# Performance work log

Hardware: AMD Instinct MI355X
Metric: run time of the kernel (lower is better)

Reference implementation:

```python
import jax, jax.numpy as jnp
import numpy as np

B, S, D, H = 2, 2048, 1280, 16
DEPTH = D // H  # 80


def setup_inputs() -> dict:
    key = jax.random.key(0)
    ks = jax.random.split(key, 6)
    scale = 1.0 / np.sqrt(D)
    x = jax.random.normal(ks[0], (B, S, D), dtype=jnp.float32)
    # causal mask: 1.0 where attention is disallowed (strict upper triangle)
    mask = jnp.triu(jnp.ones((S, S), dtype=jnp.float32), k=1)
    Wq = jax.random.normal(ks[1], (D, D), dtype=jnp.float32) * scale
    Wk = jax.random.normal(ks[2], (D, D), dtype=jnp.float32) * scale
    Wv = jax.random.normal(ks[3], (D, D), dtype=jnp.float32) * scale
    Wo = jax.random.normal(ks[4], (D, D), dtype=jnp.float32) * scale
    z = jnp.zeros((D,), dtype=jnp.float32)
    return {"x": x, "mask": mask, "Wq": Wq, "bq": z, "Wk": Wk, "bk": z,
            "Wv": Wv, "bv": z, "Wo": Wo, "bo": z}


def _split_heads(t):
    # [B, S, D] -> [B, H, S, depth]
    return t.reshape(B, -1, H, DEPTH).transpose(0, 2, 1, 3)


def reference(x, mask, Wq, bq, Wk, bk, Wv, bv, Wo, bo):
    q = _split_heads(x @ Wq + bq)
    k = _split_heads(x @ Wk + bk)
    v = _split_heads(x @ Wv + bv)
    # scaled dot-product attention with additive (masked * -10000) logits
    logits = jnp.einsum("bhqd,bhkd->bhqk", q, k) / jnp.sqrt(
        jnp.asarray(DEPTH, dtype=jnp.float32))
    logits = logits + mask * -10000.0  # mask broadcasts over [B, H]
    attn = jax.nn.softmax(logits, axis=-1)
    ctx = jnp.einsum("bhqk,bhkd->bhqd", attn, v)
    ctx = ctx.transpose(0, 2, 1, 3).reshape(B, -1, D)  # merge heads
    return ctx @ Wo + bo
```

## Files before the change

kernel.cpp:

```cpp
#include <hip/hip_runtime.h>

typedef unsigned short u16;
typedef __bf16 bf16;
typedef __bf16 bf16x8 __attribute__((ext_vector_type(8)));
typedef unsigned short u16x8 __attribute__((ext_vector_type(8)));
typedef unsigned short u16x4 __attribute__((ext_vector_type(4)));
typedef float f32x4 __attribute__((ext_vector_type(4)));

constexpr int B_ = 2, S_ = 2048, D_ = 1280, H_ = 16, DEPTH_ = 80;
constexpr int M_ = B_ * S_;
constexpr int QR_ = 128;

__device__ inline u16 f2b(float f) { return __builtin_bit_cast(u16, (bf16)f); }

typedef __attribute__((address_space(1))) const void gvoid;
typedef __attribute__((address_space(3))) void lvoid;
__device__ inline void gl_lds16(const void* g, void* l) {
  __builtin_amdgcn_global_load_lds((gvoid*)g, (lvoid*)l, 16, 0, 0);
}

__global__ __launch_bounds__(256) void prep_k(const float* __restrict__ x,
                                              u16* __restrict__ xbf,
                                              u16* __restrict__ QK,
                                              const float* __restrict__ W0,
                                              const float* __restrict__ W1,
                                              const float* __restrict__ W2,
                                              const float* __restrict__ W3,
                                              u16* __restrict__ WT) {
  __shared__ u16 t[32][33];
  int bid = blockIdx.x, tid = threadIdx.x;
  if (bid < 2560) {
    int i0 = (bid * 256 + tid) * 8;
    u16x8 v;
#pragma unroll
    for (int j = 0; j < 8; ++j) v[j] = f2b(x[i0 + j]);
    *(u16x8*)(xbf + i0) = v;
  } else if (bid < 5632) {
    int c = (bid - 2560) * 256 + tid;
    int r = c / 6, k = c - r * 6;
    u16x8 z = {};
    *(u16x8*)(QK + (size_t)r * QR_ + 80 + k * 8) = z;
  } else {
    int tt = bid - 5632;
    int z = tt / 1600, w = tt - z * 1600;
    int x0 = (w % 40) * 32, y0 = (w / 40) * 32;
    const float* srcs[4] = {W0, W1, W2, W3};
    const float* W = srcs[z];
    u16* out = WT + (size_t)z * D_ * D_;
    int tx = tid & 31, ty = tid >> 5;
#pragma unroll
    for (int i = 0; i < 4; ++i)
      t[ty + 8 * i][tx] = f2b(W[(size_t)(y0 + ty + 8 * i) * D_ + x0 + tx]);
    __syncthreads();
#pragma unroll
    for (int i = 0; i < 4; ++i)
      out[(size_t)(x0 + ty + 8 * i) * D_ + y0 + tx] = t[tx][ty + 8 * i];
  }
}

struct GemmAcc {
  f32x4 acc[4][4];
};
__device__ inline void gemm_core(const u16* __restrict__ A,
                                 const u16* __restrict__ BT, int m0, int n0,
                                 u16* a_s, u16* b_s, GemmAcc& g) {
  int tid = threadIdx.x, lane = tid & 63, wave = tid >> 6;
  int quad = lane >> 4, l15 = lane & 15;
  int wm = wave >> 1, wn = wave & 1;
  int r4 = lane >> 2, c4 = (lane & 3) * 8;

  for (int k0 = 0; k0 < D_; k0 += 32) {
    __syncthreads();
#pragma unroll
    for (int j = 0; j < 2; ++j) {
      int ch = wave * 2 + j;
      gl_lds16(A + (size_t)(m0 + ch * 16 + r4) * D_ + k0 + c4, a_s + ch * 512);
      gl_lds16(BT + (size_t)(n0 + ch * 16 + r4) * D_ + k0 + c4, b_s + ch * 512);
    }
    __syncthreads();
    bf16x8 af[4], bfr[4];
#pragma unroll
    for (int mt = 0; mt < 4; ++mt)
      af[mt] = *(const bf16x8*)(a_s + (wm * 64 + mt * 16 + l15) * 32 + quad * 8);
#pragma unroll
    for (int nt = 0; nt < 4; ++nt)
      bfr[nt] = *(const bf16x8*)(b_s + (wn * 64 + nt * 16 + l15) * 32 + quad * 8);
#pragma unroll
    for (int mt = 0; mt < 4; ++mt)
#pragma unroll
      for (int nt = 0; nt < 4; ++nt)
        g.acc[mt][nt] = __builtin_amdgcn_mfma_f32_16x16x32_bf16(
            af[mt], bfr[nt], g.acc[mt][nt], 0, 0, 0);
  }
}

__global__ __launch_bounds__(256, 4) void gemm_out(const u16* __restrict__ A,
                                                   const u16* __restrict__ BT,
                                                   const float* __restrict__ bias,
                                                   float* __restrict__ out) {
  __shared__ __align__(16) u16 a_s[128 * 32];
  __shared__ __align__(16) u16 b_s[128 * 32];
  int lane = threadIdx.x & 63, wave = threadIdx.x >> 6;
  int quad = lane >> 4, l15 = lane & 15;
  int wm = wave >> 1, wn = wave & 1;
  int m0 = blockIdx.y * 128, n0 = blockIdx.x * 128;

  GemmAcc g = {};
  gemm_core(A, BT, m0, n0, a_s, b_s, g);

#pragma unroll
  for (int nt = 0; nt < 4; ++nt) {
    int col = n0 + wn * 64 + nt * 16 + l15;
    float bv = bias[col];
#pragma unroll
    for (int mt = 0; mt < 4; ++mt)
#pragma unroll
      for (int r = 0; r < 4; ++r) {
        int row = m0 + wm * 64 + mt * 16 + quad * 4 + r;
        out[(size_t)row * D_ + col] = g.acc[mt][nt][r] + bv;
      }
  }
}

__device__ inline void stage_half(const u16* __restrict__ gsrc, int half,
                                  u16* lbase, int wave, int lane) {
  int rl = lane >> 3, c8 = lane & 7;
  int sc = (c8 ^ rl) << 3;
#pragma unroll
  for (int i = 0; i < 2; ++i) {
    int j = half * 16 + wave * 2 + i;
    gl_lds16(gsrc + (size_t)(j * 8 + rl) * D_ + sc, lbase + j * 512);
  }
}

__device__ inline bf16x8 frd(const u16* b, int r, int g) {
  return *(const bf16x8*)(b + r * 64 + ((g ^ (r & 7)) << 3));
}

__global__ __launch_bounds__(512, 2) void gemm_qkv8(
    const u16* __restrict__ A, const u16* __restrict__ BT,
    const float* __restrict__ bq, const float* __restrict__ bk,
    const float* __restrict__ bv, u16* __restrict__ Qw, u16* __restrict__ Kw,
    u16* __restrict__ Vw) {
  __shared__ __align__(16) u16 AS[2][256 * 64];
  __shared__ __align__(16) u16 BS[2][256 * 64];
  constexpr int BK = 64, NT = D_ / BK;
  int tid = threadIdx.x, lane = tid & 63, wave = tid >> 6;
  int quad = lane >> 4, l15 = lane & 15;
  int wm = wave >> 2, wn = wave & 3;
  int bid = blockIdx.x;
  int sw = (bid & 7) * 30 + (bid >> 3);
  int by = sw / 15, bx = sw - by * 15;
  int m0 = by * 256, n0 = bx * 256;
  const u16* Ab = A + (size_t)m0 * D_;
  const u16* Bb = BT + (size_t)n0 * D_;

  f32x4 acc[8][4] = {};

  stage_half(Ab, 0, (u16*)AS[0], wave, lane);
  stage_half(Ab, 1, (u16*)AS[0], wave, lane);
  stage_half(Bb, 0, (u16*)BS[0], wave, lane);
  stage_half(Bb, 1, (u16*)BS[0], wave, lane);
  stage_half(Bb + BK, 0, (u16*)BS[1], wave, lane);
  stage_half(Bb + BK, 1, (u16*)BS[1], wave, lane);
  asm volatile("s_waitcnt vmcnt(4)" ::: "memory");
  __builtin_amdgcn_s_barrier();

  bf16x8 a[4][2], bl[2][2], bh[2][2];
  int ra = wm * 128 + l15, rb = wn * 64 + l15;

#pragma unroll 2
  for (int T = 0; T < NT; ++T) {
    const u16* Ac = AS[T & 1];
    const u16* Bc = BS[T & 1];
    u16* An = (u16*)AS[(T + 1) & 1];
    u16* Bcur = (u16*)BS[T & 1];

#pragma unroll
    for (int mt = 0; mt < 4; ++mt)
#pragma unroll
      for (int kh = 0; kh < 2; ++kh)
        a[mt][kh] = frd(Ac, ra + mt * 16, kh * 4 + quad);
#pragma unroll
    for (int nt = 0; nt < 2; ++nt)
#pragma unroll
      for (int kh = 0; kh < 2; ++kh)
        bl[nt][kh] = frd(Bc, rb + nt * 16, kh * 4 + quad);
    if (T + 1 < NT) stage_half(Ab + (size_t)(T + 1) * BK, 0, An, wave, lane);
    asm volatile("" ::: "memory");
    __builtin_amdgcn_s_barrier();
    __builtin_amdgcn_s_setprio(1);
#pragma unroll
    for (int mt = 0; mt < 4; ++mt)
#pragma unroll
      for (int nt = 0; nt < 2; ++nt)
#pragma unroll
        for (int kh = 0; kh < 2; ++kh)
          acc[mt][nt] = __builtin_amdgcn_mfma_f32_16x16x32_bf16(
              a[mt][kh], bl[nt][kh], acc[mt][nt], 0, 0, 0);
    __builtin_amdgcn_s_setprio(0);
    asm volatile("" ::: "memory");
    __builtin_amdgcn_s_barrier();

#pragma unroll
    for (int nt = 0; nt < 2; ++nt)
#pragma unroll
      for (int kh = 0; kh < 2; ++kh)
        bh[nt][kh] = frd(Bc, rb + 32 + nt * 16, kh * 4 + quad);
    if (T + 1 < NT) stage_half(Ab + (size_t)(T + 1) * BK, 1, An, wave, lane);
    asm volatile("" ::: "memory");
    __builtin_amdgcn_s_barrier();
    __builtin_amdgcn_s_setprio(1);
#pragma unroll
    for (int mt = 0; mt < 4; ++mt)
#pragma unroll
      for (int nt = 0; nt < 2; ++nt)
#pragma unroll
        for (int kh = 0; kh < 2; ++kh)
          acc[mt][nt + 2] = __builtin_amdgcn_mfma_f32_16x16x32_bf16(
              a[mt][kh], bh[nt][kh], acc[mt][nt + 2], 0, 0, 0);
    __builtin_amdgcn_s_setprio(0);
    asm volatile("" ::: "memory");
    __builtin_amdgcn_s_barrier();

#pragma unroll
    for (int mt = 0; mt < 4; ++mt)
#pragma unroll
      for (int kh = 0; kh < 2; ++kh)
        a[mt][kh] = frd(Ac, ra + 64 + mt * 16, kh * 4 + quad);
    if (T + 2 < NT) stage_half(Bb + (size_t)(T + 2) * BK, 0, Bcur, wave, lane);
    asm volatile("" ::: "memory");
    __builtin_amdgcn_s_barrier();
    __builtin_amdgcn_s_setprio(1);
#pragma unroll
    for (int mt = 0; mt < 4; ++mt)
#pragma unroll
      for (int nt = 0; nt < 2; ++nt)
#pragma unroll
        for (int kh = 0; kh < 2; ++kh)
          acc[mt + 4][nt + 2] = __builtin_amdgcn_mfma_f32_16x16x32_bf16(
              a[mt][kh], bh[nt][kh], acc[mt + 4][nt + 2], 0, 0, 0);
    __builtin_amdgcn_s_setprio(0);
    asm volatile("" ::: "memory");
    __builtin_amdgcn_s_barrier();

    if (T + 2 < NT) stage_half(Bb + (size_t)(T + 2) * BK, 1, Bcur, wave, lane);
    asm volatile("" ::: "memory");
    __builtin_amdgcn_s_barrier();
    __builtin_amdgcn_s_setprio(1);
#pragma unroll
    for (int mt = 0; mt < 4; ++mt)
#pragma unroll
      for (int nt = 0; nt < 2; ++nt)
#pragma unroll
        for (int kh = 0; kh < 2; ++kh)
          acc[mt + 4][nt] = __builtin_amdgcn_mfma_f32_16x16x32_bf16(
              a[mt][kh], bl[nt][kh], acc[mt + 4][nt], 0, 0, 0);
    __builtin_amdgcn_s_setprio(0);
    if (T < NT - 2)
      asm volatile("s_waitcnt vmcnt(4)" ::: "memory");
    else if (T == NT - 2)
      asm volatile("s_waitcnt vmcnt(0)" ::: "memory");
    asm volatile("" ::: "memory");
    __builtin_amdgcn_s_barrier();
  }

  int mat = n0 / D_;
  if (mat == 2) {
#pragma unroll
    for (int nt = 0; nt < 4; ++nt) {
      int co = n0 + wn * 64 + nt * 16 + l15 - 2 * D_;
      float bb_ = bv[co];
      int h = co / DEPTH_, d = co % DEPTH_;
#pragma unroll
      for (int mt = 0; mt < 8; ++mt) {
        int row = m0 + wm * 128 + mt * 16 + quad * 4;
        int b = row >> 11, s = row & (S_ - 1);
        u16x4 pk;
#pragma unroll
        for (int r = 0; r < 4; ++r) pk[r] = f2b(acc[mt][nt][r] + bb_);
        *(u16x4*)(Vw + ((size_t)(b * H_ + h) * DEPTH_ + d) * S_ + s) = pk;
      }
    }
  } else {
    const float* bp = (mat == 0) ? bq : bk;
    u16* outp = mat ? Kw : Qw;
#pragma unroll
    for (int nt = 0; nt < 4; ++nt) {
      int co = n0 + wn * 64 + nt * 16 + l15 - mat * D_;
      float bb_ = bp[co];
      int h = co / DEPTH_, d = co % DEPTH_;
#pragma unroll
      for (int mt = 0; mt < 8; ++mt)
#pragma unroll
        for (int r = 0; r < 4; ++r) {
          int row = m0 + wm * 128 + mt * 16 + quad * 4 + r;
          int b = row >> 11, s = row & (S_ - 1);
          outp[((size_t)(b * H_ + h) * S_ + s) * QR_ + d] =
              f2b(acc[mt][nt][r] + bb_);
        }
    }
  }
}

__global__ __launch_bounds__(512, 4) void attn_k(const u16* __restrict__ Qp,
                                                 const u16* __restrict__ Kp,
                                                 const u16* __restrict__ VT,
                                                 u16* __restrict__ ctx) {
  constexpr float SCALE = 0.11180339887498949f;
  __shared__ __align__(16) u16 k_s[64 * 128];
  __shared__ __align__(16) u16 vt_s[80 * 64];
  __shared__ __align__(16) u16 p_s[128 * 72];
  int tid = threadIdx.x, lane = tid & 63, wave = tid >> 6;
  int quad = lane >> 4, l15 = lane & 15;
  int bx = blockIdx.x, by = blockIdx.y;
  int s_ = (by >> 4) & 1;
  int qt = s_ ? bx : (15 - bx);
  int bh = (by & 15) | (((by >> 5) & 1) << 4);
  const u16* Qb = Qp + (size_t)bh * S_ * QR_;
  const u16* Kb = Kp + (size_t)bh * S_ * QR_;
  const u16* Vb = VT + (size_t)bh * DEPTH_ * S_;

  bf16x8 qf[3];
#pragma unroll
  for (int ks = 0; ks < 3; ++ks)
    qf[ks] = *(const bf16x8*)(Qb + (size_t)(qt * 128 + wave * 16 + l15) * QR_ +
                              ks * 32 + quad * 8);

  f32x4 acc_o[5] = {};
  float lsum[4] = {};
  int nkt = 2 * qt + 2;

  for (int kt = 0; kt < nkt; ++kt) {
    int k0 = kt * 64;
    __syncthreads();
#pragma unroll
    for (int i = 0; i < 2; ++i) {
      int row = (wave * 2 + i) * 4 + quad;
      int sc = l15 ^ (row & 7);
      gl_lds16(Kb + (size_t)(k0 + row) * QR_ + sc * 8,
               k_s + (size_t)row * QR_ + l15 * 8);
    }
#pragma unroll
    for (int i = 0; i < 2; ++i) {
      int j = wave + 8 * i;
      if (j < 10) {
        int ch = j * 64 + lane;
        int row = ch >> 3, pos = ch & 7;
        int sc = pos ^ (row & 7);
        gl_lds16(Vb + (size_t)row * S_ + k0 + sc * 8, vt_s + ch * 8);
      }
    }
    __syncthreads();

    f32x4 sa[4] = {};
#pragma unroll
    for (int ks = 0; ks < 3; ++ks) {
      int pa = ((ks * 4 + quad) ^ (l15 & 7)) * 8;
#pragma unroll
      for (int nt = 0; nt < 4; ++nt) {
        bf16x8 bfr = *(const bf16x8*)(k_s + (size_t)(nt * 16 + l15) * QR_ + pa);
        sa[nt] = __builtin_amdgcn_mfma_f32_16x16x32_bf16(qf[ks], bfr, sa[nt], 0, 0, 0);
      }
    }
    bool diag = (kt >= 2 * qt);
#pragma unroll
    for (int nt = 0; nt < 4; ++nt)
#pragma unroll
      for (int r = 0; r < 4; ++r) {
        float p = __expf(sa[nt][r] * SCALE);
        if (diag &&
            (k0 + nt * 16 + l15) > (qt * 128 + wave * 16 + quad * 4 + r))
          p = 0.0f;
        sa[nt][r] = p;
        lsum[r] += p;
      }
    asm volatile("s_waitcnt lgkmcnt(0)" ::: "memory");
#pragma unroll
    for (int nt = 0; nt < 4; ++nt)
#pragma unroll
      for (int r = 0; r < 4; ++r)
        p_s[(wave * 16 + quad * 4 + r) * 72 + nt * 16 + l15] = f2b(sa[nt][r]);
    asm volatile("s_waitcnt lgkmcnt(0)" ::: "memory");
#pragma unroll
    for (int kk = 0; kk < 2; ++kk) {
      bf16x8 af = *(const bf16x8*)(p_s + (wave * 16 + l15) * 72 + kk * 32 + quad * 8);
#pragma unroll
      for (int d5 = 0; d5 < 5; ++d5) {
        int pv = ((kk * 4 + quad) ^ (l15 & 7)) * 8;
        bf16x8 bfr = *(const bf16x8*)(vt_s + (size_t)(d5 * 16 + l15) * 64 + pv);
        acc_o[d5] = __builtin_amdgcn_mfma_f32_16x16x32_bf16(af, bfr, acc_o[d5], 0, 0, 0);
      }
    }
  }

#pragma unroll
  for (int r = 0; r < 4; ++r)
#pragma unroll
    for (int m = 1; m < 16; m <<= 1) lsum[r] += __shfl_xor(lsum[r], m, 16);

  int b = bh >> 4, h = bh & 15;
#pragma unroll
  for (int d5 = 0; d5 < 5; ++d5)
#pragma unroll
    for (int r = 0; r < 4; ++r) {
      int s = qt * 128 + wave * 16 + quad * 4 + r;
      int col = h * DEPTH_ + d5 * 16 + l15;
      ctx[(size_t)(b * S_ + s) * D_ + col] = f2b(acc_o[d5][r] / lsum[r]);
    }
}

extern "C" void kernel_launch(void* const* d_in, const int* in_sizes, int n_in,
                              void* d_out, int out_size, void* d_ws, size_t ws_size,
                              hipStream_t stream) {
  const float* x  = (const float*)d_in[0];
  const float* Wq = (const float*)d_in[2];
  const float* bq = (const float*)d_in[3];
  const float* Wk = (const float*)d_in[4];
  const float* bk = (const float*)d_in[5];
  const float* Wv = (const float*)d_in[6];
  const float* bv = (const float*)d_in[7];
  const float* Wo = (const float*)d_in[8];
  const float* bo = (const float*)d_in[9];

  const size_t DD = (size_t)D_ * D_;
  const size_t QE = (size_t)B_ * H_ * S_ * DEPTH_;
  const size_t QP = (size_t)B_ * H_ * S_ * QR_;
  u16* xbf = (u16*)d_ws;
  u16* wT  = xbf + QE;
  u16* Qw  = wT + 4 * DD;
  u16* Kw  = Qw + QP;
  u16* Vw  = Kw + QP;
  u16* Cw  = xbf;
  size_t need = (size_t)(Vw + QE - xbf) * 2;
  if (ws_size < need) return;

  prep_k<<<12032, 256, 0, stream>>>(x, xbf, Qw, Wq, Wk, Wv, Wo, wT);
  gemm_qkv8<<<240, 512, 0, stream>>>(xbf, wT, bq, bk, bv, Qw, Kw, Vw);
  attn_k<<<dim3(8, 64), 512, 0, stream>>>(Qw, Kw, Vw, Cw);
  gemm_out<<<dim3(D_ / 128, M_ / 128), 256, 0, stream>>>(Cw, wT + 3 * DD, bo,
                                                         (float*)d_out);
}
```

Before: 271.5 us.

## Double-buffer K/V tiles and pair causal query tiles per attention block

The attention kernel now double-buffers the K and V^T tiles in LDS, issuing the async global-to-LDS loads for the next key tile before computing on the current one, so load latency overlaps the MFMA and softmax work. Each block now handles two query tiles (qt and 15-qt), giving every block the same amount of causal work, and the grid shrinks from 512 to 256 blocks. LDS use roughly doubles and the occupancy hint drops to 2 blocks per CU. Half as many blocks may leave some CUs idle.

```diff
diff --git a/kernel.cpp b/kernel.cpp
--- a/kernel.cpp
+++ b/kernel.cpp
@@ -303,111 +303,133 @@
   }
 }
 
-__global__ __launch_bounds__(512, 4) void attn_k(const u16* __restrict__ Qp,
+__device__ inline void attn_stage(const u16* __restrict__ Kb,
+                                  const u16* __restrict__ Vb, int k0, u16* ks,
+                                  u16* vs, int wave, int lane) {
+  int quad = lane >> 4, l15 = lane & 15;
+#pragma unroll
+  for (int i = 0; i < 2; ++i) {
+    int row = (wave * 2 + i) * 4 + quad;
+    int sc = l15 ^ (row & 7);
+    gl_lds16(Kb + (size_t)(k0 + row) * QR_ + sc * 8,
+             ks + (size_t)row * QR_ + l15 * 8);
+  }
+#pragma unroll
+  for (int i = 0; i < 2; ++i) {
+    int j = wave + 8 * i;
+    if (j < 10) {
+      int ch = j * 64 + lane;
+      int row = ch >> 3, pos = ch & 7;
+      int sc = pos ^ (row & 7);
+      gl_lds16(Vb + (size_t)row * S_ + k0 + sc * 8, vs + ch * 8);
+    }
+  }
+}
+
+__global__ __launch_bounds__(512, 2) void attn_k(const u16* __restrict__ Qp,
                                                  const u16* __restrict__ Kp,
                                                  const u16* __restrict__ VT,
                                                  u16* __restrict__ ctx) {
   constexpr float SCALE = 0.11180339887498949f;
-  __shared__ __align__(16) u16 k_s[64 * 128];
-  __shared__ __align__(16) u16 vt_s[80 * 64];
+  __shared__ __align__(16) u16 k_s[2][64 * 128];
+  __shared__ __align__(16) u16 vt_s[2][80 * 64];
   __shared__ __align__(16) u16 p_s[128 * 72];
   int tid = threadIdx.x, lane = tid & 63, wave = tid >> 6;
   int quad = lane >> 4, l15 = lane & 15;
-  int bx = blockIdx.x, by = blockIdx.y;
-  int s_ = (by >> 4) & 1;
-  int qt = s_ ? bx : (15 - bx);
-  int bh = (by & 15) | (((by >> 5) & 1) << 4);
+  int bid = blockIdx.x;
+  int bh = bid & 31, bx = bid >> 5;
   const u16* Qb = Qp + (size_t)bh * S_ * QR_;
   const u16* Kb = Kp + (size_t)bh * S_ * QR_;
   const u16* Vb = VT + (size_t)bh * DEPTH_ * S_;
-
-  bf16x8 qf[3];
-#pragma unroll
-  for (int ks = 0; ks < 3; ++ks)
-    qf[ks] = *(const bf16x8*)(Qb + (size_t)(qt * 128 + wave * 16 + l15) * QR_ +
-                              ks * 32 + quad * 8);
-
-  f32x4 acc_o[5] = {};
-  float lsum[4] = {};
-  int nkt = 2 * qt + 2;
-
-  for (int kt = 0; kt < nkt; ++kt) {
-    int k0 = kt * 64;
+  int b = bh >> 4, h = bh & 15;
+
+#pragma unroll 1
+  for (int t = 0; t < 2; ++t) {
+    int qt = t ? (15 - bx) : bx;
+    int nkt = 2 * qt + 2;
+
+    bf16x8 qf[3];
+#pragma unroll
+    for (int ks = 0; ks < 3; ++ks)
+      qf[ks] = *(const bf16x8*)(Qb + (size_t)(qt * 128 + wave * 16 + l15) * QR_ +
+                                ks * 32 + quad * 8);
+    f32x4 acc_o[5] = {};
+    float lsum[4] = {};
+
+    attn_stage(Kb, Vb, 0, k_s[0], vt_s[0], wave, lane);
+    asm volatile("s_waitcnt vmcnt(0)" ::: "memory");
     __syncthreads();
-#pragma unroll
-    for (int i = 0; i < 2; ++i) {
-      int row = (wave * 2 + i) * 4 + quad;
-      int sc = l15 ^ (row & 7);
-      gl_lds16(Kb + (size_t)(k0 + row) * QR_ + sc * 8,
-               k_s + (size_t)row * QR_ + l15 * 8);
-    }
-#pragma unroll
-    for (int i = 0; i < 2; ++i) {
-      int j = wave + 8 * i;
-      if (j < 10) {
-        int ch = j * 64 + lane;
-        int row = ch >> 3, pos = ch & 7;
-        int sc = pos ^ (row & 7);
-        gl_lds16(Vb + (size_t)row * S_ + k0 + sc * 8, vt_s + ch * 8);
+
+    for (int kt = 0; kt < nkt; ++kt) {
+      int k0 = kt * 64;
+      int cur = kt & 1;
+      if (kt + 1 < nkt)
+        attn_stage(Kb, Vb, k0 + 64, k_s[cur ^ 1], vt_s[cur ^ 1], wave, lane);
+      const u16* ksb = k_s[cur];
+      const u16* vsb = vt_s[cur];
+
+      f32x4 sa[4] = {};
+#pragma unroll
+      for (int ks = 0; ks < 3; ++ks) {
+        int pa = ((ks * 4 + quad) ^ (l15 & 7)) * 8;
+#pragma unroll
+        for (int nt = 0; nt < 4; ++nt) {
+          bf16x8 bfr = *(const bf16x8*)(ksb + (size_t)(nt * 16 + l15) * QR_ + pa);
+          sa[nt] =
+              __builtin_amdgcn_mfma_f32_16x16x32_bf16(qf[ks], bfr, sa[nt], 0, 0, 0);
+        }
       }
-    }
-    __syncthreads();
-
-    f32x4 sa[4] = {};
-#pragma unroll
-    for (int ks = 0; ks < 3; ++ks) {
-      int pa = ((ks * 4 + quad) ^ (l15 & 7)) * 8;
-#pragma unroll
-      for (int nt = 0; nt < 4; ++nt) {
-        bf16x8 bfr = *(const bf16x8*)(k_s + (size_t)(nt * 16 + l15) * QR_ + pa);
-        sa[nt] = __builtin_amdgcn_mfma_f32_16x16x32_bf16(qf[ks], bfr, sa[nt], 0, 0, 0);
+      bool diag = (kt >= 2 * qt);
+#pragma unroll
+      for (int nt = 0; nt < 4; ++nt)
+#pragma unroll
+        for (int r = 0; r < 4; ++r) {
+          float p = __expf(sa[nt][r] * SCALE);
+          if (diag &&
+              (k0 + nt * 16 + l15) > (qt * 128 + wave * 16 + quad * 4 + r))
+            p = 0.0f;
+          sa[nt][r] = p;
+          lsum[r] += p;
+        }
+      asm volatile("s_waitcnt lgkmcnt(0)" ::: "memory");
+#pragma unroll
+      for (int nt = 0; nt < 4; ++nt)
+#pragma unroll
+        for (int r = 0; r < 4; ++r)
+          p_s[(wave * 16 + quad * 4 + r) * 72 + nt * 16 + l15] = f2b(sa[nt][r]);
+      asm volatile("s_waitcnt lgkmcnt(0)" ::: "memory");
+#pragma unroll
+      for (int kk = 0; kk < 2; ++kk) {
+        bf16x8 af =
+            *(const bf16x8*)(p_s + (wave * 16 + l15) * 72 + kk * 32 + quad * 8);
+#pragma unroll
+        for (int d5 = 0; d5 < 5; ++d5) {
+          int pv = ((kk * 4 + quad) ^ (l15 & 7)) * 8;
+          bf16x8 bfr = *(const bf16x8*)(vsb + (size_t)(d5 * 16 + l15) * 64 + pv);
+          acc_o[d5] =
+              __builtin_amdgcn_mfma_f32_16x16x32_bf16(af, bfr, acc_o[d5], 0, 0, 0);
+        }
       }
-    }
-    bool diag = (kt >= 2 * qt);
-#pragma unroll
-    for (int nt = 0; nt < 4; ++nt)
+      asm volatile("s_waitcnt vmcnt(0)" ::: "memory");
+      __syncthreads();
+    }
+
+    float ls[4];
+#pragma unroll
+    for (int r = 0; r < 4; ++r) {
+      ls[r] = lsum[r];
+#pragma unroll
+      for (int m = 1; m < 16; m <<= 1) ls[r] += __shfl_xor(ls[r], m, 16);
+    }
+#pragma unroll
+    for (int d5 = 0; d5 < 5; ++d5)
 #pragma unroll
       for (int r = 0; r < 4; ++r) {
-        float p = __expf(sa[nt][r] * SCALE);
-        if (diag &&
-            (k0 + nt * 16 + l15) > (qt * 128 + wave * 16 + quad * 4 + r))
-          p = 0.0f;
-        sa[nt][r] = p;
-        lsum[r] += p;
+        int s = qt * 128 + wave * 16 + quad * 4 + r;
+        int col = h * DEPTH_ + d5 * 16 + l15;
+        ctx[(size_t)(b * S_ + s) * D_ + col] = f2b(acc_o[d5][r] / ls[r]);
       }
-    asm volatile("s_waitcnt lgkmcnt(0)" ::: "memory");
-#pragma unroll
-    for (int nt = 0; nt < 4; ++nt)
-#pragma unroll
-      for (int r = 0; r < 4; ++r)
-        p_s[(wave * 16 + quad * 4 + r) * 72 + nt * 16 + l15] = f2b(sa[nt][r]);
-    asm volatile("s_waitcnt lgkmcnt(0)" ::: "memory");
-#pragma unroll
-    for (int kk = 0; kk < 2; ++kk) {
-      bf16x8 af = *(const bf16x8*)(p_s + (wave * 16 + l15) * 72 + kk * 32 + quad * 8);
-#pragma unroll
-      for (int d5 = 0; d5 < 5; ++d5) {
-        int pv = ((kk * 4 + quad) ^ (l15 & 7)) * 8;
-        bf16x8 bfr = *(const bf16x8*)(vt_s + (size_t)(d5 * 16 + l15) * 64 + pv);
-        acc_o[d5] = __builtin_amdgcn_mfma_f32_16x16x32_bf16(af, bfr, acc_o[d5], 0, 0, 0);
-      }
-    }
-  }
-
-#pragma unroll
-  for (int r = 0; r < 4; ++r)
-#pragma unroll
-    for (int m = 1; m < 16; m <<= 1) lsum[r] += __shfl_xor(lsum[r], m, 16);
-
-  int b = bh >> 4, h = bh & 15;
-#pragma unroll
-  for (int d5 = 0; d5 < 5; ++d5)
-#pragma unroll
-    for (int r = 0; r < 4; ++r) {
-      int s = qt * 128 + wave * 16 + quad * 4 + r;
-      int col = h * DEPTH_ + d5 * 16 + l15;
-      ctx[(size_t)(b * S_ + s) * D_ + col] = f2b(acc_o[d5][r] / lsum[r]);
-    }
+  }
 }
 
 extern "C" void kernel_launch(void* const* d_in, const int* in_sizes, int n_in,
@@ -437,7 +459,7 @@
 
   prep_k<<<12032, 256, 0, stream>>>(x, xbf, Qw, Wq, Wk, Wv, Wo, wT);
   gemm_qkv8<<<240, 512, 0, stream>>>(xbf, wT, bq, bk, bv, Qw, Kw, Vw);
-  attn_k<<<dim3(8, 64), 512, 0, stream>>>(Qw, Kw, Vw, Cw);
+  attn_k<<<256, 512, 0, stream>>>(Qw, Kw, Vw, Cw);
   gemm_out<<<dim3(D_ / 128, M_ / 128), 256, 0, stream>>>(Cw, wT + 3 * DD, bo,
                                                          (float*)d_out);
 }
```

Result: faster. 257.0 us (-5.3%).
